# Optimization experiments

Hardware: AMD Instinct MI355X
Metric: run time of the kernel (lower is better)

Reference implementation:

```python
import jax, jax.numpy as jnp
import numpy as np

B, T, E, H = 4, 1024, 768, 12
DH = E // H
MAXP = 64  # rel_max_positions per relation type
SCALE = DH ** -0.5


def _sinusoid_embed(max_pos, dim):
    # fairseq-style sinusoid table with padding row 0 zeroed
    num = max_pos + 1
    half = dim // 2
    freq = np.exp(np.arange(half) * -(np.log(10000.0) / (half - 1)))
    ang = np.arange(num)[:, None] * freq[None, :]
    emb = np.concatenate([np.sin(ang), np.cos(ang)], axis=1)
    emb[0] = 0.0
    return jnp.asarray(emb, dtype=jnp.float32)


def _xavier(key, out_d, in_d, gain):
    bound = gain * np.sqrt(6.0 / (in_d + out_d))
    return jax.random.uniform(key, (out_d, in_d), jnp.float32, -bound, bound)


def setup_inputs() -> dict:
    key = jax.random.key(0)
    ks = jax.random.split(key, 16)
    g = 1.0 / np.sqrt(2.0)
    inp = {
        'x': jax.random.normal(ks[0], (B, T, E), jnp.float32),
        'rel_pos0': jax.random.randint(ks[1], (T, T), 0, MAXP + 1),
        'rel_pos1': jax.random.randint(ks[2], (T, T), 0, MAXP + 1),
        'rel_emb0': _sinusoid_embed(MAXP, E),
        'rel_emb1': _sinusoid_embed(MAXP, E),
    }
    names = ['Wq_r', 'Wk_r', 'Wv_r', 'Wq_s', 'Wk_s', 'Wv_s', 'Wk2', 'Wv2', 'Wrel0', 'Wrel1']
    for i, n in enumerate(names):
        inp[n] = _xavier(ks[3 + i], E, E, g)
        inp[n.replace('W', 'b', 1)] = jnp.zeros((E,), jnp.float32)
    inp['Wo'] = _xavier(ks[13], E, E, 1.0)
    inp['bo'] = jnp.zeros((E,), jnp.float32)
    return inp


def _lin(x, W, b):
    return x @ W.T + b


def _heads(x):
    return x.reshape(x.shape[0], x.shape[1], H, DH).transpose(0, 2, 1, 3)  # [B,H,T,DH]


def reference(x, rel_pos0, rel_pos1, rel_emb0, rel_emb1,
              Wq_r, bq_r, Wk_r, bk_r, Wv_r, bv_r,
              Wq_s, bq_s, Wk_s, bk_s, Wv_s, bv_s,
              Wk2, bk2, Wv2, bv2,
              Wrel0, brel0, Wrel1, brel1, Wo, bo):
    # --- sum branch: plain attention producing per-position summaries ---
    qs = _heads(_lin(x, Wq_s, bq_s)) * SCALE
    ks_ = _heads(_lin(x, Wk_s, bk_s))
    vs = _heads(_lin(x, Wv_s, bv_s))
    attn_s = jax.nn.softmax(jnp.einsum('bhqd,bhkd->bhqk', qs, ks_), axis=-1)
    sum_x = jnp.einsum('bhqk,bhkd->bhqd', attn_s, vs).transpose(0, 2, 1, 3).reshape(B, T, E)
    # summaries re-projected as extra keys/values for the reg branch
    k2 = _heads(_lin(sum_x, Wk2, bk2))
    v2 = _heads(_lin(sum_x, Wv2, bv2))
    # --- reg branch with per-relation-type RPE score biases ---
    q = _heads(_lin(x, Wq_r, bq_r)) * SCALE
    k = _heads(_lin(x, Wk_r, bk_r))
    v = _heads(_lin(x, Wv_r, bv_r))
    s_reg = jnp.einsum('bhqd,bhkd->bhqk', q, k)
    for rel_pos, rel_emb, Wr, br in ((rel_pos0, rel_emb0, Wrel0, brel0),
                                     (rel_pos1, rel_emb1, Wrel1, brel1)):
        table = _lin(rel_emb, Wr, br).reshape(-1, H, DH)       # [P,H,DH]
        ts = jnp.einsum('bhqd,phd->bhqp', q, table)            # [B,H,T,P]
        idx = jnp.broadcast_to(rel_pos[None, None], (B, H, T, T))
        s_reg = s_reg + jnp.take_along_axis(ts, idx, axis=3)   # RPE gather
    s_sum = jnp.einsum('bhqd,bhkd->bhqk', q, k2)
    attn = jax.nn.softmax(jnp.concatenate([s_reg, s_sum], axis=-1), axis=-1)  # [B,H,T,2T]
    kv = jnp.concatenate([v, v2], axis=2)                       # [B,H,2T,DH]
    out = jnp.einsum('bhqk,bhkd->bhqd', attn, kv).transpose(0, 2, 1, 3).reshape(B, T, E)
    return _lin(out, Wo, bo)
```

## Files before the change

kernel.cpp:

```cpp
#include <hip/hip_runtime.h>
#include <hip/hip_bf16.h>
#include <stdint.h>


#define DEV __device__ __forceinline__

using f32x4 = __attribute__((ext_vector_type(4))) float;
using s16x8 = __attribute__((ext_vector_type(8))) short;
using s16x4 = __attribute__((ext_vector_type(4))) short;
using i32x4 = __attribute__((ext_vector_type(4))) int;
using fvec4 = __attribute__((ext_vector_type(4))) float;
using u16 = unsigned short;

static constexpr int KD = 768;
static constexpr int PE = 4096 * 768;

DEV u16 f2bf(float f) {
  uint32_t u = __builtin_bit_cast(uint32_t, f);
  u += 0x7FFF + ((u >> 16) & 1);
  return (u16)(u >> 16);
}
DEV float bf2f(u16 h) { return __builtin_bit_cast(float, (uint32_t)h << 16); }

DEV void gload16(const void* g, void* l) {
  __builtin_amdgcn_global_load_lds((const __attribute__((address_space(1))) void*)g,
                                   (__attribute__((address_space(3))) void*)l, 16, 0, 0);
}
DEV f32x4 mfma16(s16x8 a, s16x8 b, f32x4 c) {
  return __builtin_amdgcn_mfma_f32_16x16x32_bf16(a, b, c, 0, 0, 0);
}

struct CastJobs {
  const float* src[14];
  u16* dst[14];
  int n[14];
};
__global__ __launch_bounds__(256) void cast_bf16_kernel(CastJobs J) {
  const int job = blockIdx.y;
  const int i = (blockIdx.x * 256 + threadIdx.x) * 8;
  if (i >= J.n[job]) return;
  const fvec4* s = (const fvec4*)(J.src[job] + i);
  fvec4 a = s[0], b = s[1];
  s16x8 o;
  o[0] = (short)f2bf(a[0]); o[1] = (short)f2bf(a[1]);
  o[2] = (short)f2bf(a[2]); o[3] = (short)f2bf(a[3]);
  o[4] = (short)f2bf(b[0]); o[5] = (short)f2bf(b[1]);
  o[6] = (short)f2bf(b[2]); o[7] = (short)f2bf(b[3]);
  *(s16x8*)(J.dst[job] + i) = o;
}

__global__ __launch_bounds__(256) void pack_rp_kernel(const int* rp0, const int* rp1, u16* outp) {
  const int i = (blockIdx.x * 256 + threadIdx.x) * 8;
  i32x4 a0 = *(const i32x4*)(rp0 + i), a1 = *(const i32x4*)(rp0 + i + 4);
  i32x4 b0 = *(const i32x4*)(rp1 + i), b1 = *(const i32x4*)(rp1 + i + 4);
  s16x8 o;
  o[0] = (short)(a0[0] | (b0[0] << 8));
  o[1] = (short)(a0[1] | (b0[1] << 8));
  o[2] = (short)(a0[2] | (b0[2] << 8));
  o[3] = (short)(a0[3] | (b0[3] << 8));
  o[4] = (short)(a1[0] | (b1[0] << 8));
  o[5] = (short)(a1[1] | (b1[1] << 8));
  o[6] = (short)(a1[2] | (b1[2] << 8));
  o[7] = (short)(a1[3] | (b1[3] << 8));
  *(s16x8*)(outp + i) = o;
}

struct GemmP {
  const u16* A;
  const u16* Bw;
  const float* bias[6];
  u16* out_bf;
  float* out_f;
  int epi;
};

__global__ __launch_bounds__(256) void gemm_bt(GemmP p) {
  __shared__ __align__(16) u16 As[128 * 64];
  __shared__ __align__(16) u16 Bs[128 * 64];
  const int tid = threadIdx.x;
  const int m0 = blockIdx.x * 128, n0 = blockIdx.y * 128;
  const u16* Ag = p.A + (size_t)m0 * KD;
  const u16* Bg = p.Bw + (size_t)n0 * KD;
  const int lane = tid & 63, wid = tid >> 6;
  const int wm = (wid >> 1) * 64, wn = (wid & 1) * 64;
  const int lhi = lane >> 4, llo = lane & 15;

  uint ldso[4], srco[4];
#pragma unroll
  for (int j = 0; j < 4; ++j) {
    uint o = tid * 16 + j * 4096;
    uint row = o >> 7, kc = (o >> 4) & 7;
    ldso[j] = o;
    srco[j] = row * KD + ((kc ^ (row & 7)) << 3);
  }

  f32x4 acc[4][4] = {};

  for (int kt = 0; kt < 12; ++kt) {
    const int k0 = kt * 64;
#pragma unroll
    for (int j = 0; j < 4; ++j) gload16(Ag + srco[j] + k0, (char*)As + ldso[j]);
#pragma unroll
    for (int j = 0; j < 4; ++j) gload16(Bg + srco[j] + k0, (char*)Bs + ldso[j]);
    __syncthreads();
#pragma unroll
    for (int kf = 0; kf < 2; ++kf) {
      s16x8 av[4], bv[4];
#pragma unroll
      for (int mf = 0; mf < 4; ++mf) {
        int r = wm + mf * 16 + llo;
        av[mf] = *(const s16x8*)&As[r * 64 + ((((kf << 2) | lhi) ^ (r & 7)) << 3)];
      }
#pragma unroll
      for (int nf = 0; nf < 4; ++nf) {
        int r = wn + nf * 16 + llo;
        bv[nf] = *(const s16x8*)&Bs[r * 64 + ((((kf << 2) | lhi) ^ (r & 7)) << 3)];
      }
#pragma unroll
      for (int mf = 0; mf < 4; ++mf)
#pragma unroll
        for (int nf = 0; nf < 4; ++nf)
          acc[mf][nf] = mfma16(av[mf], bv[nf], acc[mf][nf]);
    }
    __syncthreads();
  }

  const int epi = p.epi;
#pragma unroll
  for (int nf = 0; nf < 4; ++nf) {
    const int n = n0 + wn + nf * 16 + llo;
    int proj = 0, n1 = n, hh, dd;
    float bias, scale = 1.0f;
    if (epi <= 1) {
      proj = n / 768; n1 = n - proj * 768;
      hh = n1 >> 6; dd = n1 & 63;
      bias = p.bias[proj][n1];
      if (epi == 0 && (proj == 0 || proj == 3)) scale = 0.125f;
    } else {
      hh = n >> 6; dd = n & 63;
      bias = p.bias[0][n];
    }
#pragma unroll
    for (int mf = 0; mf < 4; ++mf) {
      f32x4 c = acc[mf][nf];
      const int mb = m0 + wm + mf * 16 + lhi * 4;
      if (epi == 3) {
#pragma unroll
        for (int r = 0; r < 4; ++r)
          p.out_f[(size_t)(mb + r) * 768 + n] = c[r] + bias;
      } else if (epi == 2) {
#pragma unroll
        for (int r = 0; r < 4; ++r) {
          int m = mb + r;
          if (m < 80) p.out_bf[((size_t)hh * 80 + m) * 64 + dd] = f2bf(c[r] + bias);
        }
      } else {
        const bool vlay = (epi == 0) ? (proj == 2 || proj == 5) : (proj == 1);
        if (vlay) {
          const int b = mb >> 10, t = mb & 1023;
          const int bh = b * 12 + hh;
          s16x4 o4;
          o4[0] = (short)f2bf((c[0] + bias) * scale);
          o4[1] = (short)f2bf((c[1] + bias) * scale);
          o4[2] = (short)f2bf((c[2] + bias) * scale);
          o4[3] = (short)f2bf((c[3] + bias) * scale);
          *(s16x4*)&p.out_bf[(size_t)proj * PE + ((size_t)(bh * 64 + dd)) * 1024 + t] = o4;
        } else {
#pragma unroll
          for (int r = 0; r < 4; ++r) {
            int m = mb + r;
            int b = m >> 10, t = m & 1023;
            int bh = b * 12 + hh;
            p.out_bf[(size_t)proj * PE + ((size_t)(bh * 1024 + t)) * 64 + dd] =
                f2bf((c[r] + bias) * scale);
          }
        }
      }
    }
  }
}

__global__ __launch_bounds__(256) void sum_attn_kernel(const u16* Qs, const u16* Ks,
                                                       const u16* Vst, u16* sum_x) {
  __shared__ __align__(16) u16 kbuf[64 * 64];
  __shared__ __align__(16) u16 vbuf[64 * 64];
  __shared__ __align__(16) u16 pbuf[4][16 * 72];
  const int tid = threadIdx.x, lane = tid & 63, w = tid >> 6;
  const int lhi = lane >> 4, llo = lane & 15;
  const int bid = blockIdx.x;
  const int vid = (bid & 7) * 96 + (bid >> 3);
  const int qt = vid & 15, bh = vid >> 4;
  const int qbase = qt * 64 + w * 16;

  const u16* Qg = Qs + ((size_t)bh * 1024 + qbase + llo) * 64;
  s16x8 aq0 = *(const s16x8*)(Qg + lhi * 8);
  s16x8 aq1 = *(const s16x8*)(Qg + 32 + lhi * 8);

  f32x4 accO[4] = {};
  float mrun[4], lrun[4];
#pragma unroll
  for (int r = 0; r < 4; ++r) { mrun[r] = -1e30f; lrun[r] = 0.f; }

  uint so[2], srow[2], sswz[2];
#pragma unroll
  for (int j = 0; j < 2; ++j) {
    uint o = tid * 16 + j * 4096;
    so[j] = o; srow[j] = o >> 7;
    sswz[j] = (((o >> 4) & 7) ^ (srow[j] & 7)) << 3;
  }
  const u16* Kg = Ks + (size_t)bh * 65536;
  const u16* Vg = Vst + (size_t)bh * 65536;

  for (int kt = 0; kt < 16; ++kt) {
#pragma unroll
    for (int j = 0; j < 2; ++j) {
      gload16(Kg + (size_t)kt * 4096 + srow[j] * 64 + sswz[j], (char*)kbuf + so[j]);
      gload16(Vg + (size_t)srow[j] * 1024 + kt * 64 + sswz[j], (char*)vbuf + so[j]);
    }
    __syncthreads();

    f32x4 s[4];
    __builtin_amdgcn_s_setprio(1);
#pragma unroll
    for (int kc4 = 0; kc4 < 4; ++kc4) {
      f32x4 c = {};
#pragma unroll
      for (int kf = 0; kf < 2; ++kf) {
        int kr = kc4 * 16 + llo;
        s16x8 bk = *(const s16x8*)&kbuf[kr * 64 + ((((kf << 2) | lhi) ^ (kr & 7)) << 3)];
        c = mfma16(kf ? aq1 : aq0, bk, c);
      }
      s[kc4] = c;
    }
    __builtin_amdgcn_s_setprio(0);

    float smx[4];
#pragma unroll
    for (int r = 0; r < 4; ++r)
      smx[r] = fmaxf(fmaxf(s[0][r], s[1][r]), fmaxf(s[2][r], s[3][r]));
    int ok = 1;
#pragma unroll
    for (int r = 0; r < 4; ++r) ok &= (smx[r] <= mrun[r] + 8.0f);
    if (!__all(ok)) {
#pragma unroll
      for (int msk = 1; msk < 16; msk <<= 1)
#pragma unroll
        for (int r = 0; r < 4; ++r)
          smx[r] = fmaxf(smx[r], __shfl_xor(smx[r], msk, 64));
#pragma unroll
      for (int r = 0; r < 4; ++r) {
        float mn = fmaxf(mrun[r], smx[r]);
        float corr = __expf(mrun[r] - mn);
        mrun[r] = mn;
        lrun[r] *= corr;
#pragma unroll
        for (int dc = 0; dc < 4; ++dc) accO[dc][r] *= corr;
      }
    }
#pragma unroll
    for (int r = 0; r < 4; ++r) {
      float ls = 0.f;
#pragma unroll
      for (int kc4 = 0; kc4 < 4; ++kc4) {
        float pv = __expf(s[kc4][r] - mrun[r]);
        ls += pv;
        pbuf[w][(lhi * 4 + r) * 72 + kc4 * 16 + llo] = f2bf(pv);
      }
      lrun[r] += ls;
    }

    asm volatile("s_waitcnt lgkmcnt(0)" ::: "memory");
    __builtin_amdgcn_sched_barrier(0);

    __builtin_amdgcn_s_setprio(1);
#pragma unroll
    for (int kf = 0; kf < 2; ++kf) {
      s16x8 ap = *(const s16x8*)&pbuf[w][llo * 72 + kf * 32 + lhi * 8];
#pragma unroll
      for (int dc = 0; dc < 4; ++dc) {
        int dr = dc * 16 + llo;
        s16x8 bv = *(const s16x8*)&vbuf[dr * 64 + ((((kf << 2) | lhi) ^ (dr & 7)) << 3)];
        accO[dc] = mfma16(ap, bv, accO[dc]);
      }
    }
    __builtin_amdgcn_s_setprio(0);
    __syncthreads();
  }

#pragma unroll
  for (int msk = 1; msk < 16; msk <<= 1)
#pragma unroll
    for (int r = 0; r < 4; ++r) lrun[r] += __shfl_xor(lrun[r], msk, 64);

  const int b = bh / 12, hh = bh - b * 12;
#pragma unroll
  for (int dc = 0; dc < 4; ++dc)
#pragma unroll
    for (int r = 0; r < 4; ++r) {
      int q = qbase + lhi * 4 + r;
      float o = accO[dc][r] / lrun[r];
      sum_x[((size_t)b * 1024 + q) * 768 + hh * 64 + dc * 16 + llo] = f2bf(o);
    }
}

__global__ __launch_bounds__(256) void reg_attn_kernel(
    const u16* Qr, const u16* Kr, const u16* Vrt,
    const u16* K2, const u16* V2t,
    const u16* tab0, const u16* tab1,
    const u16* rpk, u16* attn_out) {
  __shared__ __align__(16) u16 kbuf[64 * 64];
  __shared__ __align__(16) u16 vbuf[64 * 64];
  __shared__ __align__(16) u16 tsb[2][64 * 80];
  __shared__ __align__(16) u16 pbuf[4][16 * 72];
  const int tid = threadIdx.x, lane = tid & 63, w = tid >> 6;
  const int lhi = lane >> 4, llo = lane & 15;
  const int bid = blockIdx.x;
  const int vid = (bid & 7) * 96 + (bid >> 3);
  const int qt = vid & 15, bh = vid >> 4;
  const int b = bh / 12, hh = bh - b * 12;
  const int qbase = qt * 64 + w * 16;

  const u16* Qg = Qr + ((size_t)bh * 1024 + qbase + llo) * 64;
  s16x8 aq0 = *(const s16x8*)(Qg + lhi * 8);
  s16x8 aq1 = *(const s16x8*)(Qg + 32 + lhi * 8);

#pragma unroll
  for (int tt = 0; tt < 2; ++tt) {
    const u16* tb = tt ? tab1 : tab0;
#pragma unroll
    for (int pf = 0; pf < 5; ++pf) {
      f32x4 c = {};
#pragma unroll
      for (int kf = 0; kf < 2; ++kf) {
        s16x8 bt = *(const s16x8*)(tb + ((size_t)hh * 80 + pf * 16 + llo) * 64 + kf * 32 + lhi * 8);
        c = mfma16(kf ? aq1 : aq0, bt, c);
      }
#pragma unroll
      for (int r = 0; r < 4; ++r)
        tsb[tt][(w * 16 + lhi * 4 + r) * 80 + pf * 16 + llo] = f2bf(c[r]);
    }
  }
  __syncthreads();

  f32x4 accO[4] = {};
  float mrun[4], lrun[4];
#pragma unroll
  for (int r = 0; r < 4; ++r) { mrun[r] = -1e30f; lrun[r] = 0.f; }

  int tbase[4];
#pragma unroll
  for (int r = 0; r < 4; ++r) tbase[r] = (w * 16 + lhi * 4 + r) * 80;

  uint so[2], srow[2], sswz[2];
#pragma unroll
  for (int j = 0; j < 2; ++j) {
    uint o = tid * 16 + j * 4096;
    so[j] = o; srow[j] = o >> 7;
    sswz[j] = (((o >> 4) & 7) ^ (srow[j] & 7)) << 3;
  }
  const u16* KgA = Kr + (size_t)bh * 65536;
  const u16* KgB = K2 + (size_t)bh * 65536;
  const u16* VgA = Vrt + (size_t)bh * 65536;
  const u16* VgB = V2t + (size_t)bh * 65536;

  auto tile = [&](const u16* Kg, const u16* Vg, int kk, bool gather) {
#pragma unroll
    for (int j = 0; j < 2; ++j) {
      gload16(Kg + (size_t)kk * 4096 + srow[j] * 64 + sswz[j], (char*)kbuf + so[j]);
      gload16(Vg + (size_t)srow[j] * 1024 + kk * 64 + sswz[j], (char*)vbuf + so[j]);
    }
    u16 pp[16];
    if (gather) {
#pragma unroll
      for (int kc4 = 0; kc4 < 4; ++kc4)
#pragma unroll
        for (int r = 0; r < 4; ++r)
          pp[kc4 * 4 + r] =
              rpk[(size_t)(qbase + lhi * 4 + r) * 1024 + kk * 64 + kc4 * 16 + llo];
    }
    __syncthreads();

    f32x4 s[4];
    __builtin_amdgcn_s_setprio(1);
#pragma unroll
    for (int kc4 = 0; kc4 < 4; ++kc4) {
      f32x4 c = {};
#pragma unroll
      for (int kf = 0; kf < 2; ++kf) {
        int kr = kc4 * 16 + llo;
        s16x8 bk = *(const s16x8*)&kbuf[kr * 64 + ((((kf << 2) | lhi) ^ (kr & 7)) << 3)];
        c = mfma16(kf ? aq1 : aq0, bk, c);
      }
      s[kc4] = c;
    }
    __builtin_amdgcn_s_setprio(0);

    if (gather) {
#pragma unroll
      for (int kc4 = 0; kc4 < 4; ++kc4)
#pragma unroll
        for (int r = 0; r < 4; ++r) {
          u16 v = pp[kc4 * 4 + r];
          s[kc4][r] += bf2f(tsb[0][tbase[r] + (v & 255)]) + bf2f(tsb[1][tbase[r] + (v >> 8)]);
        }
    }

    float smx[4];
#pragma unroll
    for (int r = 0; r < 4; ++r)
      smx[r] = fmaxf(fmaxf(s[0][r], s[1][r]), fmaxf(s[2][r], s[3][r]));
    int ok = 1;
#pragma unroll
    for (int r = 0; r < 4; ++r) ok &= (smx[r] <= mrun[r] + 8.0f);
    if (!__all(ok)) {
#pragma unroll
      for (int msk = 1; msk < 16; msk <<= 1)
#pragma unroll
        for (int r = 0; r < 4; ++r)
          smx[r] = fmaxf(smx[r], __shfl_xor(smx[r], msk, 64));
#pragma unroll
      for (int r = 0; r < 4; ++r) {
        float mn = fmaxf(mrun[r], smx[r]);
        float corr = __expf(mrun[r] - mn);
        mrun[r] = mn;
        lrun[r] *= corr;
#pragma unroll
        for (int dc = 0; dc < 4; ++dc) accO[dc][r] *= corr;
      }
    }
#pragma unroll
    for (int r = 0; r < 4; ++r) {
      float ls = 0.f;
#pragma unroll
      for (int kc4 = 0; kc4 < 4; ++kc4) {
        float pv = __expf(s[kc4][r] - mrun[r]);
        ls += pv;
        pbuf[w][(lhi * 4 + r) * 72 + kc4 * 16 + llo] = f2bf(pv);
      }
      lrun[r] += ls;
    }

    asm volatile("s_waitcnt lgkmcnt(0)" ::: "memory");
    __builtin_amdgcn_sched_barrier(0);

    __builtin_amdgcn_s_setprio(1);
#pragma unroll
    for (int kf = 0; kf < 2; ++kf) {
      s16x8 ap = *(const s16x8*)&pbuf[w][llo * 72 + kf * 32 + lhi * 8];
#pragma unroll
      for (int dc = 0; dc < 4; ++dc) {
        int dr = dc * 16 + llo;
        s16x8 bv = *(const s16x8*)&vbuf[dr * 64 + ((((kf << 2) | lhi) ^ (dr & 7)) << 3)];
        accO[dc] = mfma16(ap, bv, accO[dc]);
      }
    }
    __builtin_amdgcn_s_setprio(0);
    __syncthreads();
  };

  for (int kt = 0; kt < 16; ++kt) tile(KgA, VgA, kt, true);
  for (int kt = 0; kt < 16; ++kt) tile(KgB, VgB, kt, false);

#pragma unroll
  for (int msk = 1; msk < 16; msk <<= 1)
#pragma unroll
    for (int r = 0; r < 4; ++r) lrun[r] += __shfl_xor(lrun[r], msk, 64);

#pragma unroll
  for (int dc = 0; dc < 4; ++dc)
#pragma unroll
    for (int r = 0; r < 4; ++r) {
      int q = qbase + lhi * 4 + r;
      float o = accO[dc][r] / lrun[r];
      attn_out[((size_t)b * 1024 + q) * 768 + hh * 64 + dc * 16 + llo] = f2bf(o);
    }
}

extern "C" void kernel_launch(void* const* d_in, const int* in_sizes, int n_in,
                              void* d_out, int out_size, void* d_ws, size_t ws_size,
                              hipStream_t stream) {
  (void)in_sizes; (void)n_in; (void)out_size; (void)ws_size;
  const float* x     = (const float*)d_in[0];
  const int*   rp0   = (const int*)d_in[1];
  const int*   rp1   = (const int*)d_in[2];
  const float* re0   = (const float*)d_in[3];
  const float* re1   = (const float*)d_in[4];
  const float* Wq_r  = (const float*)d_in[5];  const float* bq_r = (const float*)d_in[6];
  const float* Wk_r  = (const float*)d_in[7];  const float* bk_r = (const float*)d_in[8];
  const float* Wv_r  = (const float*)d_in[9];  const float* bv_r = (const float*)d_in[10];
  const float* Wq_s  = (const float*)d_in[11]; const float* bq_s = (const float*)d_in[12];
  const float* Wk_s  = (const float*)d_in[13]; const float* bk_s = (const float*)d_in[14];
  const float* Wv_s  = (const float*)d_in[15]; const float* bv_s = (const float*)d_in[16];
  const float* Wk2   = (const float*)d_in[17]; const float* bk2  = (const float*)d_in[18];
  const float* Wv2   = (const float*)d_in[19]; const float* bv2  = (const float*)d_in[20];
  const float* Wrel0 = (const float*)d_in[21]; const float* brel0 = (const float*)d_in[22];
  const float* Wrel1 = (const float*)d_in[23]; const float* brel1 = (const float*)d_in[24];
  const float* Wo    = (const float*)d_in[25]; const float* bo   = (const float*)d_in[26];
  float* out = (float*)d_out;

  char* wp = (char*)d_ws;
  auto carve = [&](size_t bytes) {
    char* r = wp;
    wp += (bytes + 255) & ~(size_t)255;
    return r;
  };
  u16* xb     = (u16*)carve((size_t)PE * 2);
  u16* Wcat1  = (u16*)carve((size_t)4608 * 768 * 2);
  u16* Wcat2  = (u16*)carve((size_t)1536 * 768 * 2);
  u16* Wrel0b = (u16*)carve((size_t)768 * 768 * 2);
  u16* Wrel1b = (u16*)carve((size_t)768 * 768 * 2);
  u16* Wob    = (u16*)carve((size_t)768 * 768 * 2);
  u16* relA0  = (u16*)carve((size_t)128 * 768 * 2);
  u16* relA1  = (u16*)carve((size_t)128 * 768 * 2);
  u16* qkv    = (u16*)carve((size_t)6 * PE * 2);
  u16* k2v2   = (u16*)carve((size_t)2 * PE * 2);
  u16* tb0    = (u16*)carve((size_t)12 * 80 * 64 * 2);
  u16* tb1    = (u16*)carve((size_t)12 * 80 * 64 * 2);
  u16* rpk    = (u16*)carve((size_t)1024 * 1024 * 2);
  u16* sumx   = (u16*)carve((size_t)PE * 2);
  u16* aout   = (u16*)carve((size_t)PE * 2);

  const int wn_ = 768 * 768;
  CastJobs J;
  const float* srcs[14] = {x, Wq_r, Wk_r, Wv_r, Wq_s, Wk_s, Wv_s, Wk2, Wv2, Wrel0, Wrel1, Wo, re0, re1};
  u16* dsts[14] = {xb, Wcat1, Wcat1 + wn_, Wcat1 + 2 * wn_, Wcat1 + 3 * wn_, Wcat1 + 4 * wn_,
                   Wcat1 + 5 * wn_, Wcat2, Wcat2 + wn_, Wrel0b, Wrel1b, Wob, relA0, relA1};
  int ns[14] = {PE, wn_, wn_, wn_, wn_, wn_, wn_, wn_, wn_, wn_, wn_, wn_, 65 * 768, 65 * 768};
  for (int i = 0; i < 14; ++i) { J.src[i] = srcs[i]; J.dst[i] = dsts[i]; J.n[i] = ns[i]; }
  cast_bf16_kernel<<<dim3(1536, 14), 256, 0, stream>>>(J);

  pack_rp_kernel<<<dim3(512), 256, 0, stream>>>(rp0, rp1, rpk);

  GemmP g1{};
  g1.A = xb; g1.Bw = Wcat1;
  g1.bias[0] = bq_r; g1.bias[1] = bk_r; g1.bias[2] = bv_r;
  g1.bias[3] = bq_s; g1.bias[4] = bk_s; g1.bias[5] = bv_s;
  g1.out_bf = qkv; g1.epi = 0;
  gemm_bt<<<dim3(32, 36), 256, 0, stream>>>(g1);

  GemmP gt0{}; gt0.A = relA0; gt0.Bw = Wrel0b; gt0.bias[0] = brel0; gt0.out_bf = tb0; gt0.epi = 2;
  gemm_bt<<<dim3(1, 6), 256, 0, stream>>>(gt0);
  GemmP gt1{}; gt1.A = relA1; gt1.Bw = Wrel1b; gt1.bias[0] = brel1; gt1.out_bf = tb1; gt1.epi = 2;
  gemm_bt<<<dim3(1, 6), 256, 0, stream>>>(gt1);

  sum_attn_kernel<<<dim3(768), 256, 0, stream>>>(qkv + (size_t)3 * PE, qkv + (size_t)4 * PE,
                                                 qkv + (size_t)5 * PE, sumx);

  GemmP g2{};
  g2.A = sumx; g2.Bw = Wcat2; g2.bias[0] = bk2; g2.bias[1] = bv2;
  g2.out_bf = k2v2; g2.epi = 1;
  gemm_bt<<<dim3(32, 12), 256, 0, stream>>>(g2);

  reg_attn_kernel<<<dim3(768), 256, 0, stream>>>(qkv, qkv + (size_t)PE, qkv + (size_t)2 * PE,
                                                 k2v2, k2v2 + (size_t)PE, tb0, tb1, rpk, aout);

  GemmP gf{};
  gf.A = aout; gf.Bw = Wob; gf.bias[0] = bo; gf.out_f = out; gf.epi = 3;
  gemm_bt<<<dim3(32, 6), 256, 0, stream>>>(gf);
}
```

Baseline: 386.5 us.

## Transpose attention score MFMA, fold log2e into Q scale, merge rel-table GEMMs

Swaps the MFMA operand order so each lane holds one query row's scores across keys. This turns per-row softmax max/sum reductions into two cross-lane shuffles instead of four. Folds log2(e) into the Q scaling constant so softmax can use exp2f, and packs probabilities with v_cvt_pk_bf16_f32 into vectorized LDS stores. The two relative-position table GEMMs become one launch via blockIdx.z, and the RPE index loads are vectorized. The trade-off is extra shuffles to broadcast per-row correction and normalizer values back to the output layout.

```diff
diff --git a/kernel.cpp b/kernel.cpp
--- a/kernel.cpp
+++ b/kernel.cpp
@@ -9,11 +9,13 @@
 using s16x8 = __attribute__((ext_vector_type(8))) short;
 using s16x4 = __attribute__((ext_vector_type(4))) short;
 using i32x4 = __attribute__((ext_vector_type(4))) int;
+using u32x2 = __attribute__((ext_vector_type(2))) unsigned int;
 using fvec4 = __attribute__((ext_vector_type(4))) float;
 using u16 = unsigned short;
 
 static constexpr int KD = 768;
 static constexpr int PE = 4096 * 768;
+static constexpr float QSCL = 0.18033688011112042f;
 
 DEV u16 f2bf(float f) {
   uint32_t u = __builtin_bit_cast(uint32_t, f);
@@ -21,6 +23,11 @@
   return (u16)(u >> 16);
 }
 DEV float bf2f(u16 h) { return __builtin_bit_cast(float, (uint32_t)h << 16); }
+DEV unsigned int cvtpk(float a, float b) {
+  unsigned int r;
+  asm("v_cvt_pk_bf16_f32 %0, %1, %2" : "=v"(r) : "v"(a), "v"(b));
+  return r;
+}
 
 DEV void gload16(const void* g, void* l) {
   __builtin_amdgcn_global_load_lds((const __attribute__((address_space(1))) void*)g,
@@ -71,6 +78,9 @@
   const float* bias[6];
   u16* out_bf;
   float* out_f;
+  const u16* A2;
+  const u16* Bw2;
+  u16* out2;
   int epi;
 };
 
@@ -79,8 +89,9 @@
   __shared__ __align__(16) u16 Bs[128 * 64];
   const int tid = threadIdx.x;
   const int m0 = blockIdx.x * 128, n0 = blockIdx.y * 128;
-  const u16* Ag = p.A + (size_t)m0 * KD;
-  const u16* Bg = p.Bw + (size_t)n0 * KD;
+  const int zz = blockIdx.z;
+  const u16* Ag = (zz ? p.A2 : p.A) + (size_t)m0 * KD;
+  const u16* Bg = (zz ? p.Bw2 : p.Bw) + (size_t)n0 * KD;
   const int lane = tid & 63, wid = tid >> 6;
   const int wm = (wid >> 1) * 64, wn = (wid & 1) * 64;
   const int lhi = lane >> 4, llo = lane & 15;
@@ -135,10 +146,10 @@
       proj = n / 768; n1 = n - proj * 768;
       hh = n1 >> 6; dd = n1 & 63;
       bias = p.bias[proj][n1];
-      if (epi == 0 && (proj == 0 || proj == 3)) scale = 0.125f;
+      if (epi == 0 && (proj == 0 || proj == 3)) scale = QSCL;
     } else {
       hh = n >> 6; dd = n & 63;
-      bias = p.bias[0][n];
+      bias = p.bias[zz ? 1 : 0][n];
     }
 #pragma unroll
     for (int mf = 0; mf < 4; ++mf) {
@@ -149,10 +160,11 @@
         for (int r = 0; r < 4; ++r)
           p.out_f[(size_t)(mb + r) * 768 + n] = c[r] + bias;
       } else if (epi == 2) {
+        u16* ob = zz ? p.out2 : p.out_bf;
 #pragma unroll
         for (int r = 0; r < 4; ++r) {
           int m = mb + r;
-          if (m < 80) p.out_bf[((size_t)hh * 80 + m) * 64 + dd] = f2bf(c[r] + bias);
+          if (m < 80) ob[((size_t)hh * 80 + m) * 64 + dd] = f2bf(c[r] + bias);
         }
       } else {
         const bool vlay = (epi == 0) ? (proj == 2 || proj == 5) : (proj == 1);
@@ -197,9 +209,7 @@
   s16x8 aq1 = *(const s16x8*)(Qg + 32 + lhi * 8);
 
   f32x4 accO[4] = {};
-  float mrun[4], lrun[4];
-#pragma unroll
-  for (int r = 0; r < 4; ++r) { mrun[r] = -1e30f; lrun[r] = 0.f; }
+  float mrun = -1e30f, lrun = 0.f;
 
   uint so[2], srow[2], sswz[2];
 #pragma unroll
@@ -228,49 +238,42 @@
       for (int kf = 0; kf < 2; ++kf) {
         int kr = kc4 * 16 + llo;
         s16x8 bk = *(const s16x8*)&kbuf[kr * 64 + ((((kf << 2) | lhi) ^ (kr & 7)) << 3)];
-        c = mfma16(kf ? aq1 : aq0, bk, c);
+        c = mfma16(bk, kf ? aq1 : aq0, c);
       }
       s[kc4] = c;
     }
     __builtin_amdgcn_s_setprio(0);
 
-    float smx[4];
-#pragma unroll
-    for (int r = 0; r < 4; ++r)
-      smx[r] = fmaxf(fmaxf(s[0][r], s[1][r]), fmaxf(s[2][r], s[3][r]));
-    int ok = 1;
-#pragma unroll
-    for (int r = 0; r < 4; ++r) ok &= (smx[r] <= mrun[r] + 8.0f);
-    if (!__all(ok)) {
-#pragma unroll
-      for (int msk = 1; msk < 16; msk <<= 1)
-#pragma unroll
-        for (int r = 0; r < 4; ++r)
-          smx[r] = fmaxf(smx[r], __shfl_xor(smx[r], msk, 64));
-#pragma unroll
-      for (int r = 0; r < 4; ++r) {
-        float mn = fmaxf(mrun[r], smx[r]);
-        float corr = __expf(mrun[r] - mn);
-        mrun[r] = mn;
-        lrun[r] *= corr;
-#pragma unroll
-        for (int dc = 0; dc < 4; ++dc) accO[dc][r] *= corr;
-      }
-    }
-#pragma unroll
-    for (int r = 0; r < 4; ++r) {
-      float ls = 0.f;
-#pragma unroll
-      for (int kc4 = 0; kc4 < 4; ++kc4) {
-        float pv = __expf(s[kc4][r] - mrun[r]);
-        ls += pv;
-        pbuf[w][(lhi * 4 + r) * 72 + kc4 * 16 + llo] = f2bf(pv);
-      }
-      lrun[r] += ls;
-    }
-
-    asm volatile("s_waitcnt lgkmcnt(0)" ::: "memory");
-    __builtin_amdgcn_sched_barrier(0);
+    float smx = s[0][0];
+#pragma unroll
+    for (int kc4 = 0; kc4 < 4; ++kc4)
+#pragma unroll
+      for (int r = 0; r < 4; ++r) smx = fmaxf(smx, s[kc4][r]);
+    if (!__all(smx <= mrun + 8.0f)) {
+      float mall = fmaxf(smx, __shfl_xor(smx, 16, 64));
+      mall = fmaxf(mall, __shfl_xor(mall, 32, 64));
+      float mn = fmaxf(mrun, mall);
+      float corr = exp2f(mrun - mn);
+      mrun = mn;
+      lrun *= corr;
+      float cf[4];
+#pragma unroll
+      for (int r = 0; r < 4; ++r) cf[r] = __shfl(corr, lhi * 4 + r, 64);
+#pragma unroll
+      for (int dc = 0; dc < 4; ++dc)
+#pragma unroll
+        for (int r = 0; r < 4; ++r) accO[dc][r] *= cf[r];
+    }
+    float ls = 0.f;
+#pragma unroll
+    for (int kc4 = 0; kc4 < 4; ++kc4) {
+      float p0 = exp2f(s[kc4][0] - mrun), p1 = exp2f(s[kc4][1] - mrun);
+      float p2 = exp2f(s[kc4][2] - mrun), p3 = exp2f(s[kc4][3] - mrun);
+      ls += (p0 + p1) + (p2 + p3);
+      u32x2 pk; pk[0] = cvtpk(p0, p1); pk[1] = cvtpk(p2, p3);
+      *(u32x2*)&pbuf[w][llo * 72 + kc4 * 16 + lhi * 4] = pk;
+    }
+    lrun += ls;
 
     __builtin_amdgcn_s_setprio(1);
 #pragma unroll
@@ -287,10 +290,11 @@
     __syncthreads();
   }
 
-#pragma unroll
-  for (int msk = 1; msk < 16; msk <<= 1)
-#pragma unroll
-    for (int r = 0; r < 4; ++r) lrun[r] += __shfl_xor(lrun[r], msk, 64);
+  lrun += __shfl_xor(lrun, 16, 64);
+  lrun += __shfl_xor(lrun, 32, 64);
+  float linv[4];
+#pragma unroll
+  for (int r = 0; r < 4; ++r) linv[r] = 1.0f / __shfl(lrun, lhi * 4 + r, 64);
 
   const int b = bh / 12, hh = bh - b * 12;
 #pragma unroll
@@ -298,8 +302,7 @@
 #pragma unroll
     for (int r = 0; r < 4; ++r) {
       int q = qbase + lhi * 4 + r;
-      float o = accO[dc][r] / lrun[r];
-      sum_x[((size_t)b * 1024 + q) * 768 + hh * 64 + dc * 16 + llo] = f2bf(o);
+      sum_x[((size_t)b * 1024 + q) * 768 + hh * 64 + dc * 16 + llo] = f2bf(accO[dc][r] * linv[r]);
     }
 }
 
@@ -310,7 +313,8 @@
     const u16* rpk, u16* attn_out) {
   __shared__ __align__(16) u16 kbuf[64 * 64];
   __shared__ __align__(16) u16 vbuf[64 * 64];
-  __shared__ __align__(16) u16 tsb[2][64 * 80];
+  __shared__ __align__(16) u16 tsb0[64 * 80];
+  __shared__ __align__(16) u16 tsb1[64 * 80];
   __shared__ __align__(16) u16 pbuf[4][16 * 72];
   const int tid = threadIdx.x, lane = tid & 63, w = tid >> 6;
   const int lhi = lane >> 4, llo = lane & 15;
@@ -319,6 +323,7 @@
   const int qt = vid & 15, bh = vid >> 4;
   const int b = bh / 12, hh = bh - b * 12;
   const int qbase = qt * 64 + w * 16;
+  const int qloc = w * 16 + llo;
 
   const u16* Qg = Qr + ((size_t)bh * 1024 + qbase + llo) * 64;
   s16x8 aq0 = *(const s16x8*)(Qg + lhi * 8);
@@ -327,29 +332,23 @@
 #pragma unroll
   for (int tt = 0; tt < 2; ++tt) {
     const u16* tb = tt ? tab1 : tab0;
+    u16* dst = tt ? tsb1 : tsb0;
 #pragma unroll
     for (int pf = 0; pf < 5; ++pf) {
       f32x4 c = {};
 #pragma unroll
       for (int kf = 0; kf < 2; ++kf) {
         s16x8 bt = *(const s16x8*)(tb + ((size_t)hh * 80 + pf * 16 + llo) * 64 + kf * 32 + lhi * 8);
-        c = mfma16(kf ? aq1 : aq0, bt, c);
-      }
-#pragma unroll
-      for (int r = 0; r < 4; ++r)
-        tsb[tt][(w * 16 + lhi * 4 + r) * 80 + pf * 16 + llo] = f2bf(c[r]);
+        c = mfma16(bt, kf ? aq1 : aq0, c);
+      }
+      u32x2 pk; pk[0] = cvtpk(c[0], c[1]); pk[1] = cvtpk(c[2], c[3]);
+      *(u32x2*)&dst[(w * 16 + llo) * 80 + pf * 16 + lhi * 4] = pk;
     }
   }
   __syncthreads();
 
   f32x4 accO[4] = {};
-  float mrun[4], lrun[4];
-#pragma unroll
-  for (int r = 0; r < 4; ++r) { mrun[r] = -1e30f; lrun[r] = 0.f; }
-
-  int tbase[4];
-#pragma unroll
-  for (int r = 0; r < 4; ++r) tbase[r] = (w * 16 + lhi * 4 + r) * 80;
+  float mrun = -1e30f, lrun = 0.f;
 
   uint so[2], srow[2], sswz[2];
 #pragma unroll
@@ -369,14 +368,11 @@
       gload16(Kg + (size_t)kk * 4096 + srow[j] * 64 + sswz[j], (char*)kbuf + so[j]);
       gload16(Vg + (size_t)srow[j] * 1024 + kk * 64 + sswz[j], (char*)vbuf + so[j]);
     }
-    u16 pp[16];
+    s16x4 pp4[4];
     if (gather) {
 #pragma unroll
       for (int kc4 = 0; kc4 < 4; ++kc4)
-#pragma unroll
-        for (int r = 0; r < 4; ++r)
-          pp[kc4 * 4 + r] =
-              rpk[(size_t)(qbase + lhi * 4 + r) * 1024 + kk * 64 + kc4 * 16 + llo];
+        pp4[kc4] = *(const s16x4*)&rpk[(size_t)(qbase + llo) * 1024 + kk * 64 + kc4 * 16 + lhi * 4];
     }
     __syncthreads();
 
@@ -389,7 +385,7 @@
       for (int kf = 0; kf < 2; ++kf) {
         int kr = kc4 * 16 + llo;
         s16x8 bk = *(const s16x8*)&kbuf[kr * 64 + ((((kf << 2) | lhi) ^ (kr & 7)) << 3)];
-        c = mfma16(kf ? aq1 : aq0, bk, c);
+        c = mfma16(bk, kf ? aq1 : aq0, c);
       }
       s[kc4] = c;
     }
@@ -400,48 +396,41 @@
       for (int kc4 = 0; kc4 < 4; ++kc4)
 #pragma unroll
         for (int r = 0; r < 4; ++r) {
-          u16 v = pp[kc4 * 4 + r];
-          s[kc4][r] += bf2f(tsb[0][tbase[r] + (v & 255)]) + bf2f(tsb[1][tbase[r] + (v >> 8)]);
+          int v = (u16)pp4[kc4][r];
+          s[kc4][r] += bf2f(tsb0[qloc * 80 + (v & 255)]) + bf2f(tsb1[qloc * 80 + (v >> 8)]);
         }
     }
 
-    float smx[4];
-#pragma unroll
-    for (int r = 0; r < 4; ++r)
-      smx[r] = fmaxf(fmaxf(s[0][r], s[1][r]), fmaxf(s[2][r], s[3][r]));
-    int ok = 1;
-#pragma unroll
-    for (int r = 0; r < 4; ++r) ok &= (smx[r] <= mrun[r] + 8.0f);
-    if (!__all(ok)) {
-#pragma unroll
-      for (int msk = 1; msk < 16; msk <<= 1)
-#pragma unroll
-        for (int r = 0; r < 4; ++r)
-          smx[r] = fmaxf(smx[r], __shfl_xor(smx[r], msk, 64));
-#pragma unroll
-      for (int r = 0; r < 4; ++r) {
-        float mn = fmaxf(mrun[r], smx[r]);
-        float corr = __expf(mrun[r] - mn);
-        mrun[r] = mn;
-        lrun[r] *= corr;
-#pragma unroll
-        for (int dc = 0; dc < 4; ++dc) accO[dc][r] *= corr;
-      }
-    }
-#pragma unroll
-    for (int r = 0; r < 4; ++r) {
-      float ls = 0.f;
-#pragma unroll
-      for (int kc4 = 0; kc4 < 4; ++kc4) {
-        float pv = __expf(s[kc4][r] - mrun[r]);
-        ls += pv;
-        pbuf[w][(lhi * 4 + r) * 72 + kc4 * 16 + llo] = f2bf(pv);
-      }
-      lrun[r] += ls;
-    }
-
-    asm volatile("s_waitcnt lgkmcnt(0)" ::: "memory");
-    __builtin_amdgcn_sched_barrier(0);
+    float smx = s[0][0];
+#pragma unroll
+    for (int kc4 = 0; kc4 < 4; ++kc4)
+#pragma unroll
+      for (int r = 0; r < 4; ++r) smx = fmaxf(smx, s[kc4][r]);
+    if (!__all(smx <= mrun + 8.0f)) {
+      float mall = fmaxf(smx, __shfl_xor(smx, 16, 64));
+      mall = fmaxf(mall, __shfl_xor(mall, 32, 64));
+      float mn = fmaxf(mrun, mall);
+      float corr = exp2f(mrun - mn);
+      mrun = mn;
+      lrun *= corr;
+      float cf[4];
+#pragma unroll
+      for (int r = 0; r < 4; ++r) cf[r] = __shfl(corr, lhi * 4 + r, 64);
+#pragma unroll
+      for (int dc = 0; dc < 4; ++dc)
+#pragma unroll
+        for (int r = 0; r < 4; ++r) accO[dc][r] *= cf[r];
+    }
+    float ls = 0.f;
+#pragma unroll
+    for (int kc4 = 0; kc4 < 4; ++kc4) {
+      float p0 = exp2f(s[kc4][0] - mrun), p1 = exp2f(s[kc4][1] - mrun);
+      float p2 = exp2f(s[kc4][2] - mrun), p3 = exp2f(s[kc4][3] - mrun);
+      ls += (p0 + p1) + (p2 + p3);
+      u32x2 pk; pk[0] = cvtpk(p0, p1); pk[1] = cvtpk(p2, p3);
+      *(u32x2*)&pbuf[w][llo * 72 + kc4 * 16 + lhi * 4] = pk;
+    }
+    lrun += ls;
 
     __builtin_amdgcn_s_setprio(1);
 #pragma unroll
@@ -461,18 +450,18 @@
   for (int kt = 0; kt < 16; ++kt) tile(KgA, VgA, kt, true);
   for (int kt = 0; kt < 16; ++kt) tile(KgB, VgB, kt, false);
 
-#pragma unroll
-  for (int msk = 1; msk < 16; msk <<= 1)
-#pragma unroll
-    for (int r = 0; r < 4; ++r) lrun[r] += __shfl_xor(lrun[r], msk, 64);
+  lrun += __shfl_xor(lrun, 16, 64);
+  lrun += __shfl_xor(lrun, 32, 64);
+  float linv[4];
+#pragma unroll
+  for (int r = 0; r < 4; ++r) linv[r] = 1.0f / __shfl(lrun, lhi * 4 + r, 64);
 
 #pragma unroll
   for (int dc = 0; dc < 4; ++dc)
 #pragma unroll
     for (int r = 0; r < 4; ++r) {
       int q = qbase + lhi * 4 + r;
-      float o = accO[dc][r] / lrun[r];
-      attn_out[((size_t)b * 1024 + q) * 768 + hh * 64 + dc * 16 + llo] = f2bf(o);
+      attn_out[((size_t)b * 1024 + q) * 768 + hh * 64 + dc * 16 + llo] = f2bf(accO[dc][r] * linv[r]);
     }
 }
 
@@ -538,10 +527,11 @@
   g1.out_bf = qkv; g1.epi = 0;
   gemm_bt<<<dim3(32, 36), 256, 0, stream>>>(g1);
 
-  GemmP gt0{}; gt0.A = relA0; gt0.Bw = Wrel0b; gt0.bias[0] = brel0; gt0.out_bf = tb0; gt0.epi = 2;
-  gemm_bt<<<dim3(1, 6), 256, 0, stream>>>(gt0);
-  GemmP gt1{}; gt1.A = relA1; gt1.Bw = Wrel1b; gt1.bias[0] = brel1; gt1.out_bf = tb1; gt1.epi = 2;
-  gemm_bt<<<dim3(1, 6), 256, 0, stream>>>(gt1);
+  GemmP gt{};
+  gt.A = relA0; gt.Bw = Wrel0b; gt.bias[0] = brel0; gt.out_bf = tb0;
+  gt.A2 = relA1; gt.Bw2 = Wrel1b; gt.bias[1] = brel1; gt.out2 = tb1;
+  gt.epi = 2;
+  gemm_bt<<<dim3(1, 6, 2), 256, 0, stream>>>(gt);
 
   sum_attn_kernel<<<dim3(768), 256, 0, stream>>>(qkv + (size_t)3 * PE, qkv + (size_t)4 * PE,
                                                  qkv + (size_t)5 * PE, sumx);
```

Measured after the change: 366.3 us. -5.2%, faster.
